# Kernel optimization log

Measured on AMD Instinct MI355X. Metric: run time of the kernel, lower is better.

## Reference

```python
import jax, jax.numpy as jnp
import numpy as np

NEG_INF = -1e9  # Keras uses a large negative for masked logits


def setup_inputs() -> dict:
    key = jax.random.key(0)
    k1, k2, k3, k4, k5 = jax.random.split(key, 5)
    B, Tq, Tv, D, U = 8, 128, 128, 512, 1024
    query = jax.random.normal(k1, (B, Tq, D), dtype=jnp.float32)
    value = jax.random.normal(k2, (B, Tv, D), dtype=jnp.float32)
    mask = jnp.ones((B, Tv), dtype=bool)
    # Dense(units, use_bias=False) kernels and AdditiveAttention scale vector
    W1 = jax.random.normal(k3, (D, U), dtype=jnp.float32) * (1.0 / np.sqrt(D))
    W2 = jax.random.normal(k4, (D, U), dtype=jnp.float32) * (1.0 / np.sqrt(D))
    scale = jax.random.normal(k5, (U,), dtype=jnp.float32) * (1.0 / np.sqrt(U))
    return {"query": query, "value": value, "mask": mask,
            "W1": W1, "W2": W2, "scale": scale}


def reference(query, value, mask, W1, W2, scale):
    # Projections (Dense, no bias)
    wq = jnp.einsum('btd,du->btu', query, W1)   # [B, Tq, U]
    wk = jnp.einsum('bsd,du->bsu', value, W2)   # [B, Tv, U]
    # Additive (Bahdanau) scores: sum_u scale_u * tanh(wq + wk)
    # Materializes [B, Tq, Tv, U] broadcast-add like Keras AdditiveAttention.
    scores = jnp.einsum('u,btsu->bts', scale,
                        jnp.tanh(wq[:, :, None, :] + wk[:, None, :, :]))
    # value mask over key axis (query_mask is all-ones in the source -> no-op)
    scores = jnp.where(mask[:, None, :], scores, NEG_INF)
    attn = jax.nn.softmax(scores, axis=-1)       # [B, Tq, Tv]
    context = jnp.einsum('bts,bsd->btd', attn, value)  # [B, Tq, D]
    return context, attn
```

## Files before the change

kernel.cpp:

```cpp
#include <hip/hip_runtime.h>

#define B_  8
#define TQ  128
#define TV  128
#define DIM 512
#define UU  1024
#define NSPLIT 8
#define NP  (B_ * TQ * TV)
#define C2  2.885390081777927f

__global__ __launch_bounds__(256) void k_proj(
    const float* __restrict__ Q, const float* __restrict__ Vv,
    const float* __restrict__ W1, const float* __restrict__ W2,
    float* __restrict__ Eq, float* __restrict__ Ek)
{
    const int N = UU, K = DIM;
    const float* A = blockIdx.z ? Vv : Q;
    const float* W = blockIdx.z ? W2 : W1;
    float*       C = blockIdx.z ? Ek : Eq;

    __shared__ float As[32][68];
    __shared__ float Bs[32][68];

    const int tid  = threadIdx.x;
    const int tx   = tid & 15;
    const int ty   = tid >> 4;
    const int row0 = blockIdx.y * 64;
    const int col0 = blockIdx.x * 64;

    const int a_m  = tid >> 2;
    const int a_kq = tid & 3;
    const int b_n4 = (tid & 15) * 4;
    const int b_k  = tid >> 4;

    float acc[4][4] = {};

    for (int kt = 0; kt < K; kt += 32) {
        const float* ap = &A[(row0 + a_m) * K + kt + a_kq * 8];
        float4 a0 = *(const float4*)ap;
        float4 a1 = *(const float4*)(ap + 4);
        As[a_kq * 8 + 0][a_m] = a0.x;
        As[a_kq * 8 + 1][a_m] = a0.y;
        As[a_kq * 8 + 2][a_m] = a0.z;
        As[a_kq * 8 + 3][a_m] = a0.w;
        As[a_kq * 8 + 4][a_m] = a1.x;
        As[a_kq * 8 + 5][a_m] = a1.y;
        As[a_kq * 8 + 6][a_m] = a1.z;
        As[a_kq * 8 + 7][a_m] = a1.w;
        #pragma unroll
        for (int h = 0; h < 2; ++h) {
            int k = b_k + h * 16;
            *(float4*)&Bs[k][b_n4] = *(const float4*)&W[(kt + k) * N + col0 + b_n4];
        }
        __syncthreads();
        #pragma unroll
        for (int k = 0; k < 32; ++k) {
            float4 a = *(const float4*)&As[k][ty * 4];
            float4 b = *(const float4*)&Bs[k][tx * 4];
            float af[4] = {a.x, a.y, a.z, a.w};
            float bf[4] = {b.x, b.y, b.z, b.w};
            #pragma unroll
            for (int i = 0; i < 4; ++i)
                #pragma unroll
                for (int j = 0; j < 4; ++j)
                    acc[i][j] = fmaf(af[i], bf[j], acc[i][j]);
        }
        __syncthreads();
    }
    #pragma unroll
    for (int i = 0; i < 4; ++i) {
        float4 o;
        o.x = __builtin_amdgcn_exp2f(C2 * acc[i][0]);
        o.y = __builtin_amdgcn_exp2f(C2 * acc[i][1]);
        o.z = __builtin_amdgcn_exp2f(C2 * acc[i][2]);
        o.w = __builtin_amdgcn_exp2f(C2 * acc[i][3]);
        *(float4*)&C[(row0 + ty * 4 + i) * N + col0 + tx * 4] = o;
    }
}

__global__ __launch_bounds__(256) void k_scores(
    const float* __restrict__ Eq, const float* __restrict__ Ek,
    const float* __restrict__ scale, float* __restrict__ part)
{
    __shared__ float qs[32][132];
    __shared__ float ks[32][132];
    __shared__ float ss[128];

    const int tid = threadIdx.x;
    const int tx  = tid & 15;
    const int ty  = tid >> 4;
    const int b   = blockIdx.z & 7;
    const int us  = blockIdx.z >> 3;
    const int t0  = blockIdx.y * 32;
    const int s0  = blockIdx.x * 32;
    const int u0  = us * (UU / NSPLIT);

    {
        const int c = (tid & 31) * 4;
        const int r0 = tid >> 5;
        #pragma unroll
        for (int i = 0; i < 4; ++i) {
            int r = r0 + i * 8;
            *(float4*)&qs[r][c] = *(const float4*)&Eq[(b * TQ + t0 + r) * UU + u0 + c];
            *(float4*)&ks[r][c] = *(const float4*)&Ek[(b * TV + s0 + r) * UU + u0 + c];
        }
        if (tid < 32)
            *(float4*)&ss[tid * 4] = *(const float4*)&scale[u0 + tid * 4];
    }
    __syncthreads();

    float a00 = 0.f, a01 = 0.f, a10 = 0.f, a11 = 0.f;

    #pragma unroll 4
    for (int u4 = 0; u4 < 32; ++u4) {
        float4 q0 = *(const float4*)&qs[ty][u4 * 4];
        float4 q1 = *(const float4*)&qs[ty + 16][u4 * 4];
        float4 k0 = *(const float4*)&ks[tx][u4 * 4];
        float4 k1 = *(const float4*)&ks[tx + 16][u4 * 4];
        float4 sv = *(const float4*)&ss[u4 * 4];

        #define PAIR(ACC, QV, KV)                                           \
        {                                                                   \
            float p1 = QV.x * KV.x, p2 = QV.y * KV.y;                       \
            float b1 = p1 + 1.f,   b2 = p2 + 1.f;                           \
            float n1 = fmaf(sv.y, b1, sv.x * b2);                           \
            ACC = fmaf(n1, __builtin_amdgcn_rcpf(b1 * b2), ACC);            \
            float p3 = QV.z * KV.z, p4 = QV.w * KV.w;                       \
            float b3 = p3 + 1.f,   b4 = p4 + 1.f;                           \
            float n2 = fmaf(sv.w, b3, sv.z * b4);                           \
            ACC = fmaf(n2, __builtin_amdgcn_rcpf(b3 * b4), ACC);            \
        }
        PAIR(a00, q0, k0)
        PAIR(a01, q0, k1)
        PAIR(a10, q1, k0)
        PAIR(a11, q1, k1)
        #undef PAIR
    }

    const int t = t0 + ty, s = s0 + tx;
    float* p = &part[us * NP + (b * TQ + t) * TV + s];
    p[0]            = a00;
    p[16]           = a01;
    p[16 * TV]      = a10;
    p[16 * TV + 16] = a11;
}

__global__ __launch_bounds__(256) void k_softmax(
    const float* __restrict__ part, const int* __restrict__ mask,
    float* __restrict__ attn)
{
    const int tid  = threadIdx.x;
    const int wave = tid >> 6;
    const int lane = tid & 63;
    const int row  = blockIdx.x * 4 + wave;
    const int b    = row >> 7;
    const int base = row * TV;

    float p0 = 0.f, p1 = 0.f;
    #pragma unroll
    for (int i = 0; i < NSPLIT; ++i) {
        p0 += part[i * NP + base + lane];
        p1 += part[i * NP + base + lane + 64];
    }
    float x0 = -2.f * p0, x1 = -2.f * p1;
    if (!mask[b * TV + lane])      x0 = -1e9f;
    if (!mask[b * TV + lane + 64]) x1 = -1e9f;

    float m = fmaxf(x0, x1);
    #pragma unroll
    for (int o = 32; o > 0; o >>= 1) m = fmaxf(m, __shfl_xor(m, o, 64));
    const float L2E = 1.4426950408889634f;
    float e0 = __builtin_amdgcn_exp2f((x0 - m) * L2E);
    float e1 = __builtin_amdgcn_exp2f((x1 - m) * L2E);
    float s = e0 + e1;
    #pragma unroll
    for (int o = 32; o > 0; o >>= 1) s += __shfl_xor(s, o, 64);
    float r = __builtin_amdgcn_rcpf(s);
    attn[base + lane]      = e0 * r;
    attn[base + lane + 64] = e1 * r;
}

__global__ __launch_bounds__(256) void k_context(
    const float* __restrict__ attn, const float* __restrict__ Vv,
    float* __restrict__ ctx)
{
    __shared__ float at[128][20];

    const int tid = threadIdx.x;
    const int b   = blockIdx.z;
    const int tt  = blockIdx.y;
    const int dc  = blockIdx.x;
    {
        int tl = tid & 15;
        int s0 = (tid >> 4) * 8;
        const float* src = &attn[(b * TQ + tt * 16 + tl) * TV + s0];
        float4 a0 = *(const float4*)src;
        float4 a1 = *(const float4*)(src + 4);
        at[s0 + 0][tl] = a0.x; at[s0 + 1][tl] = a0.y;
        at[s0 + 2][tl] = a0.z; at[s0 + 3][tl] = a0.w;
        at[s0 + 4][tl] = a1.x; at[s0 + 5][tl] = a1.y;
        at[s0 + 6][tl] = a1.z; at[s0 + 7][tl] = a1.w;
    }
    __syncthreads();

    const int d  = (tid & 127) + dc * 128;
    const int tg = tid >> 7;
    float acc[8] = {};
    const float* vp = &Vv[b * TV * DIM + d];
    for (int s = 0; s < TV; ++s) {
        float v = vp[s * DIM];
        float4 a0 = *(const float4*)&at[s][tg * 8];
        float4 a1 = *(const float4*)&at[s][tg * 8 + 4];
        acc[0] = fmaf(a0.x, v, acc[0]);
        acc[1] = fmaf(a0.y, v, acc[1]);
        acc[2] = fmaf(a0.z, v, acc[2]);
        acc[3] = fmaf(a0.w, v, acc[3]);
        acc[4] = fmaf(a1.x, v, acc[4]);
        acc[5] = fmaf(a1.y, v, acc[5]);
        acc[6] = fmaf(a1.z, v, acc[6]);
        acc[7] = fmaf(a1.w, v, acc[7]);
    }
    #pragma unroll
    for (int j = 0; j < 8; ++j) {
        int t = tt * 16 + tg * 8 + j;
        ctx[(b * TQ + t) * DIM + d] = acc[j];
    }
}

extern "C" void kernel_launch(void* const* d_in, const int* in_sizes, int n_in,
                              void* d_out, int out_size, void* d_ws, size_t ws_size,
                              hipStream_t stream)
{
    const float* query = (const float*)d_in[0];
    const float* value = (const float*)d_in[1];
    const int*   mask  = (const int*)d_in[2];
    const float* W1    = (const float*)d_in[3];
    const float* W2    = (const float*)d_in[4];
    const float* scale = (const float*)d_in[5];

    float* out  = (float*)d_out;
    float* ctx  = out;
    float* attn = out + B_ * TQ * DIM;

    float* Eq   = (float*)d_ws;
    float* Ek   = Eq + 1024 * 1024;
    float* part = Ek + 1024 * 1024;

    hipLaunchKernelGGL(k_proj,    dim3(16, 16, 2),        dim3(256), 0, stream,
                       query, value, W1, W2, Eq, Ek);
    hipLaunchKernelGGL(k_scores,  dim3(4, 4, 8 * NSPLIT), dim3(256), 0, stream,
                       Eq, Ek, scale, part);
    hipLaunchKernelGGL(k_softmax, dim3(256),              dim3(256), 0, stream,
                       part, mask, attn);
    hipLaunchKernelGGL(k_context, dim3(4, 8, 8),          dim3(256), 0, stream,
                       attn, value, ctx);
}
```

Measured before the change: 130.2 us.

## Run projection GEMM on bf16 MFMA with split hi/lo precision emulation

Replaces the FP32 FMA tiled projection GEMM with MFMA 16x16x32 bf16 instructions. Three bf16x3 products (hi*hi, hi*lo, lo*hi) approximate FP32 accuracy. Two new prep kernels split the inputs into hi/lo bf16 halves, and the weights are also transposed to K-major. This aims to cut the FP32 GEMM compute cost, at the price of two extra launches, extra workspace traffic, and a small accuracy loss.

```diff
diff --git a/kernel.cpp b/kernel.cpp
--- a/kernel.cpp
+++ b/kernel.cpp
@@ -9,74 +9,154 @@
 #define NP  (B_ * TQ * TV)
 #define C2  2.885390081777927f
 
+typedef __attribute__((ext_vector_type(8))) short     short8;
+typedef __attribute__((ext_vector_type(4))) float     f32x4;
+typedef __attribute__((ext_vector_type(4))) unsigned short us4;
+
+__device__ __forceinline__ unsigned short bf16_rtne(float x) {
+    unsigned u = __float_as_uint(x);
+    unsigned r = u + 0x7FFF + ((u >> 16) & 1);
+    return (unsigned short)(r >> 16);
+}
+__device__ __forceinline__ float bf16_to_f(unsigned short h) {
+    return __uint_as_float(((unsigned)h) << 16);
+}
+
+__global__ __launch_bounds__(256) void k_prep_a(
+    const float* __restrict__ Q, const float* __restrict__ Vv,
+    unsigned short* __restrict__ Ah, unsigned short* __restrict__ Al)
+{
+    int idx = blockIdx.x * 256 + threadIdx.x;
+    int mat = idx >> 17;
+    const float* src = mat ? Vv : Q;
+    int off = (idx & 131071) * 4;
+    float4 v = *(const float4*)&src[off];
+    us4 h, l;
+    h.x = bf16_rtne(v.x); l.x = bf16_rtne(v.x - bf16_to_f(h.x));
+    h.y = bf16_rtne(v.y); l.y = bf16_rtne(v.y - bf16_to_f(h.y));
+    h.z = bf16_rtne(v.z); l.z = bf16_rtne(v.z - bf16_to_f(h.z));
+    h.w = bf16_rtne(v.w); l.w = bf16_rtne(v.w - bf16_to_f(h.w));
+    *(us4*)&Ah[mat * 524288 + off] = h;
+    *(us4*)&Al[mat * 524288 + off] = l;
+}
+
+__global__ __launch_bounds__(256) void k_prep_w(
+    const float* __restrict__ W1, const float* __restrict__ W2,
+    unsigned short* __restrict__ Wh, unsigned short* __restrict__ Wl)
+{
+    __shared__ float ts[32][36];
+    const int t   = threadIdx.x;
+    const int mat = blockIdx.z;
+    const int n0  = blockIdx.x * 32;
+    const int k0  = blockIdx.y * 32;
+    const float* W = mat ? W2 : W1;
+
+    int kk = t >> 3, n4 = (t & 7) * 4;
+    float4 w = *(const float4*)&W[(k0 + kk) * UU + n0 + n4];
+    ts[n4 + 0][kk] = w.x; ts[n4 + 1][kk] = w.y;
+    ts[n4 + 2][kk] = w.z; ts[n4 + 3][kk] = w.w;
+    __syncthreads();
+
+    int nn = t >> 3, k4 = (t & 7) * 4;
+    float4 v = *(const float4*)&ts[nn][k4];
+    us4 h, l;
+    h.x = bf16_rtne(v.x); l.x = bf16_rtne(v.x - bf16_to_f(h.x));
+    h.y = bf16_rtne(v.y); l.y = bf16_rtne(v.y - bf16_to_f(h.y));
+    h.z = bf16_rtne(v.z); l.z = bf16_rtne(v.z - bf16_to_f(h.z));
+    h.w = bf16_rtne(v.w); l.w = bf16_rtne(v.w - bf16_to_f(h.w));
+    unsigned off = mat * 524288 + (n0 + nn) * 512 + k0 + k4;
+    *(us4*)&Wh[off] = h;
+    *(us4*)&Wl[off] = l;
+}
+
+#define PK 40
 __global__ __launch_bounds__(256) void k_proj(
-    const float* __restrict__ Q, const float* __restrict__ Vv,
-    const float* __restrict__ W1, const float* __restrict__ W2,
+    const unsigned short* __restrict__ Ah, const unsigned short* __restrict__ Al,
+    const unsigned short* __restrict__ Bh, const unsigned short* __restrict__ Bl,
     float* __restrict__ Eq, float* __restrict__ Ek)
 {
-    const int N = UU, K = DIM;
-    const float* A = blockIdx.z ? Vv : Q;
-    const float* W = blockIdx.z ? W2 : W1;
-    float*       C = blockIdx.z ? Ek : Eq;
-
-    __shared__ float As[32][68];
-    __shared__ float Bs[32][68];
+    __shared__ short sAh[64 * PK], sAl[64 * PK], sBh[64 * PK], sBl[64 * PK];
 
     const int tid  = threadIdx.x;
-    const int tx   = tid & 15;
-    const int ty   = tid >> 4;
-    const int row0 = blockIdx.y * 64;
-    const int col0 = blockIdx.x * 64;
-
-    const int a_m  = tid >> 2;
-    const int a_kq = tid & 3;
-    const int b_n4 = (tid & 15) * 4;
-    const int b_k  = tid >> 4;
-
-    float acc[4][4] = {};
-
-    for (int kt = 0; kt < K; kt += 32) {
-        const float* ap = &A[(row0 + a_m) * K + kt + a_kq * 8];
-        float4 a0 = *(const float4*)ap;
-        float4 a1 = *(const float4*)(ap + 4);
-        As[a_kq * 8 + 0][a_m] = a0.x;
-        As[a_kq * 8 + 1][a_m] = a0.y;
-        As[a_kq * 8 + 2][a_m] = a0.z;
-        As[a_kq * 8 + 3][a_m] = a0.w;
-        As[a_kq * 8 + 4][a_m] = a1.x;
-        As[a_kq * 8 + 5][a_m] = a1.y;
-        As[a_kq * 8 + 6][a_m] = a1.z;
-        As[a_kq * 8 + 7][a_m] = a1.w;
-        #pragma unroll
-        for (int h = 0; h < 2; ++h) {
-            int k = b_k + h * 16;
-            *(float4*)&Bs[k][b_n4] = *(const float4*)&W[(kt + k) * N + col0 + b_n4];
-        }
+    const int wave = tid >> 6;
+    const int lane = tid & 63;
+    const int mat  = blockIdx.z;
+    const int m0   = blockIdx.y * 64;
+    const int n0   = blockIdx.x * 64;
+
+    const unsigned mb = mat * 524288u;
+    const int wm = (wave & 1) * 32;
+    const int wn = (wave >> 1) * 32;
+
+    const int sm = tid >> 2, sg = tid & 3;
+    const unsigned short* gAh = Ah + mb + (m0 + sm) * 512 + sg * 8;
+    const unsigned short* gAl = Al + mb + (m0 + sm) * 512 + sg * 8;
+    const unsigned short* gBh = Bh + mb + (n0 + sm) * 512 + sg * 8;
+    const unsigned short* gBl = Bl + mb + (n0 + sm) * 512 + sg * 8;
+    const int sOff = sm * PK + sg * 8;
+
+    const int fr = lane & 15, fq = lane >> 4;
+    const int aOff0 = (wm + fr) * PK + fq * 8;
+    const int aOff1 = (wm + 16 + fr) * PK + fq * 8;
+    const int bOff0 = (wn + fr) * PK + fq * 8;
+    const int bOff1 = (wn + 16 + fr) * PK + fq * 8;
+
+    f32x4 acc00 = {0.f, 0.f, 0.f, 0.f};
+    f32x4 acc01 = {0.f, 0.f, 0.f, 0.f};
+    f32x4 acc10 = {0.f, 0.f, 0.f, 0.f};
+    f32x4 acc11 = {0.f, 0.f, 0.f, 0.f};
+
+    for (int kc = 0; kc < 16; ++kc) {
+        int4 vah = *(const int4*)(gAh + kc * 32);
+        int4 val = *(const int4*)(gAl + kc * 32);
+        int4 vbh = *(const int4*)(gBh + kc * 32);
+        int4 vbl = *(const int4*)(gBl + kc * 32);
+        *(int4*)&sAh[sOff] = vah;
+        *(int4*)&sAl[sOff] = val;
+        *(int4*)&sBh[sOff] = vbh;
+        *(int4*)&sBl[sOff] = vbl;
         __syncthreads();
-        #pragma unroll
-        for (int k = 0; k < 32; ++k) {
-            float4 a = *(const float4*)&As[k][ty * 4];
-            float4 b = *(const float4*)&Bs[k][tx * 4];
-            float af[4] = {a.x, a.y, a.z, a.w};
-            float bf[4] = {b.x, b.y, b.z, b.w};
-            #pragma unroll
-            for (int i = 0; i < 4; ++i)
-                #pragma unroll
-                for (int j = 0; j < 4; ++j)
-                    acc[i][j] = fmaf(af[i], bf[j], acc[i][j]);
-        }
+
+        short8 a0h = *(const short8*)&sAh[aOff0];
+        short8 a0l = *(const short8*)&sAl[aOff0];
+        short8 a1h = *(const short8*)&sAh[aOff1];
+        short8 a1l = *(const short8*)&sAl[aOff1];
+        short8 b0h = *(const short8*)&sBh[bOff0];
+        short8 b0l = *(const short8*)&sBl[bOff0];
+        short8 b1h = *(const short8*)&sBh[bOff1];
+        short8 b1l = *(const short8*)&sBl[bOff1];
+
+        acc00 = __builtin_amdgcn_mfma_f32_16x16x32_bf16(a0h, b0h, acc00, 0, 0, 0);
+        acc00 = __builtin_amdgcn_mfma_f32_16x16x32_bf16(a0h, b0l, acc00, 0, 0, 0);
+        acc00 = __builtin_amdgcn_mfma_f32_16x16x32_bf16(a0l, b0h, acc00, 0, 0, 0);
+
+        acc01 = __builtin_amdgcn_mfma_f32_16x16x32_bf16(a0h, b1h, acc01, 0, 0, 0);
+        acc01 = __builtin_amdgcn_mfma_f32_16x16x32_bf16(a0h, b1l, acc01, 0, 0, 0);
+        acc01 = __builtin_amdgcn_mfma_f32_16x16x32_bf16(a0l, b1h, acc01, 0, 0, 0);
+
+        acc10 = __builtin_amdgcn_mfma_f32_16x16x32_bf16(a1h, b0h, acc10, 0, 0, 0);
+        acc10 = __builtin_amdgcn_mfma_f32_16x16x32_bf16(a1h, b0l, acc10, 0, 0, 0);
+        acc10 = __builtin_amdgcn_mfma_f32_16x16x32_bf16(a1l, b0h, acc10, 0, 0, 0);
+
+        acc11 = __builtin_amdgcn_mfma_f32_16x16x32_bf16(a1h, b1h, acc11, 0, 0, 0);
+        acc11 = __builtin_amdgcn_mfma_f32_16x16x32_bf16(a1h, b1l, acc11, 0, 0, 0);
+        acc11 = __builtin_amdgcn_mfma_f32_16x16x32_bf16(a1l, b1h, acc11, 0, 0, 0);
         __syncthreads();
     }
-    #pragma unroll
-    for (int i = 0; i < 4; ++i) {
-        float4 o;
-        o.x = __builtin_amdgcn_exp2f(C2 * acc[i][0]);
-        o.y = __builtin_amdgcn_exp2f(C2 * acc[i][1]);
-        o.z = __builtin_amdgcn_exp2f(C2 * acc[i][2]);
-        o.w = __builtin_amdgcn_exp2f(C2 * acc[i][3]);
-        *(float4*)&C[(row0 + ty * 4 + i) * N + col0 + tx * 4] = o;
-    }
-}
+
+    float* C = mat ? Ek : Eq;
+    #pragma unroll
+    for (int r = 0; r < 4; ++r) {
+        int row0 = m0 + wm + fq * 4 + r;
+        int row1 = row0 + 16;
+        int col0 = n0 + wn + fr;
+        C[row0 * UU + col0]      = __builtin_amdgcn_exp2f(C2 * acc00[r]);
+        C[row0 * UU + col0 + 16] = __builtin_amdgcn_exp2f(C2 * acc01[r]);
+        C[row1 * UU + col0]      = __builtin_amdgcn_exp2f(C2 * acc10[r]);
+        C[row1 * UU + col0 + 16] = __builtin_amdgcn_exp2f(C2 * acc11[r]);
+    }
+}
+#undef PK
 
 __global__ __launch_bounds__(256) void k_scores(
     const float* __restrict__ Eq, const float* __restrict__ Ek,
@@ -96,7 +176,7 @@
     const int u0  = us * (UU / NSPLIT);
 
     {
-        const int c = (tid & 31) * 4;
+        const int c  = (tid & 31) * 4;
         const int r0 = tid >> 5;
         #pragma unroll
         for (int i = 0; i < 4; ++i) {
@@ -245,13 +325,21 @@
     float* Eq   = (float*)d_ws;
     float* Ek   = Eq + 1024 * 1024;
     float* part = Ek + 1024 * 1024;
-
-    hipLaunchKernelGGL(k_proj,    dim3(16, 16, 2),        dim3(256), 0, stream,
-                       query, value, W1, W2, Eq, Ek);
-    hipLaunchKernelGGL(k_scores,  dim3(4, 4, 8 * NSPLIT), dim3(256), 0, stream,
+    unsigned short* Ah = (unsigned short*)(part + NSPLIT * NP);
+    unsigned short* Al = Ah + 2 * 1024 * 512;
+    unsigned short* Wh = Al + 2 * 1024 * 512;
+    unsigned short* Wl = Wh + 2 * 1024 * 512;
+
+    hipLaunchKernelGGL(k_prep_a, dim3(1024),       dim3(256), 0, stream,
+                       query, value, Ah, Al);
+    hipLaunchKernelGGL(k_prep_w, dim3(32, 16, 2),  dim3(256), 0, stream,
+                       W1, W2, Wh, Wl);
+    hipLaunchKernelGGL(k_proj,   dim3(16, 16, 2),  dim3(256), 0, stream,
+                       Ah, Al, Wh, Wl, Eq, Ek);
+    hipLaunchKernelGGL(k_scores, dim3(4, 4, 8 * NSPLIT), dim3(256), 0, stream,
                        Eq, Ek, scale, part);
-    hipLaunchKernelGGL(k_softmax, dim3(256),              dim3(256), 0, stream,
+    hipLaunchKernelGGL(k_softmax, dim3(256),       dim3(256), 0, stream,
                        part, mask, attn);
-    hipLaunchKernelGGL(k_context, dim3(4, 8, 8),          dim3(256), 0, stream,
+    hipLaunchKernelGGL(k_context, dim3(4, 8, 8),   dim3(256), 0, stream,
                        attn, value, ctx);
 }
```

Measured after the change: 117.5 us. -9.7%, faster.
